# Kernel optimization log

Measured on AMD Instinct MI355X. Metric: run time of the kernel, lower is better.

Reference implementation:

```python
import jax, jax.numpy as jnp
import numpy as np

ALPHA = 0.1
NUM_CLASSES = 1000
B, D = 16384, 2048


def setup_inputs() -> dict:
    key = jax.random.key(0)
    k1, k2 = jax.random.split(key)
    x = jax.random.normal(k1, (B, D), dtype=jnp.float32)
    y = jax.random.randint(k2, (B,), 0, NUM_CLASSES)
    return {"x": x, "y": y}


def reference(x, y):
    # Per-class mean/std via a single segment reduction (equivalent to the
    # original masked loop over classes; torch .std(0) is unbiased, ddof=1).
    cnt = jax.ops.segment_sum(jnp.ones((x.shape[0],), x.dtype), y, num_segments=NUM_CLASSES)  # [C]
    s = jax.ops.segment_sum(x, y, num_segments=NUM_CLASSES)        # [C, D]
    sq = jax.ops.segment_sum(x * x, y, num_segments=NUM_CLASSES)   # [C, D]
    cnt_ = cnt[:, None]
    mean = s / cnt_
    var = (sq - cnt_ * mean * mean) / (cnt_ - 1.0)  # unbiased variance
    std = jnp.sqrt(jnp.maximum(var, 0.0))
    nk, pk = jax.random.split(jax.random.key(42))
    # torch.normal(mean, std).detach()
    class_noise = jax.lax.stop_gradient(mean + std * jax.random.normal(nk, mean.shape, x.dtype))
    index = jax.random.permutation(pk, x.shape[0])
    newY = y[index]
    out = (1.0 - ALPHA) * x + ALPHA * class_noise[newY]
    return out, newY
```

## Files before the change

### kernel.cpp

```cpp
#include <hip/hip_runtime.h>
#include <cstdint>
#include <cstddef>

#define B_ROWS 16384
#define D_COLS 2048
#define NCLS   1000

__host__ __device__ __forceinline__ uint32_t rotl32(uint32_t v, int r) {
    return (v << r) | (v >> (32 - r));
}

__host__ __device__ inline void tf2x32(uint32_t k0, uint32_t k1,
                                       uint32_t x0, uint32_t x1,
                                       uint32_t& o0, uint32_t& o1) {
    uint32_t ks0 = k0, ks1 = k1, ks2 = k0 ^ k1 ^ 0x1BD11BDAu;
    x0 += ks0; x1 += ks1;
    x0 += x1; x1 = rotl32(x1, 13); x1 ^= x0;
    x0 += x1; x1 = rotl32(x1, 15); x1 ^= x0;
    x0 += x1; x1 = rotl32(x1, 26); x1 ^= x0;
    x0 += x1; x1 = rotl32(x1, 6);  x1 ^= x0;
    x0 += ks1; x1 += ks2 + 1u;
    x0 += x1; x1 = rotl32(x1, 17); x1 ^= x0;
    x0 += x1; x1 = rotl32(x1, 29); x1 ^= x0;
    x0 += x1; x1 = rotl32(x1, 16); x1 ^= x0;
    x0 += x1; x1 = rotl32(x1, 24); x1 ^= x0;
    x0 += ks2; x1 += ks0 + 2u;
    x0 += x1; x1 = rotl32(x1, 13); x1 ^= x0;
    x0 += x1; x1 = rotl32(x1, 15); x1 ^= x0;
    x0 += x1; x1 = rotl32(x1, 26); x1 ^= x0;
    x0 += x1; x1 = rotl32(x1, 6);  x1 ^= x0;
    x0 += ks0; x1 += ks1 + 3u;
    x0 += x1; x1 = rotl32(x1, 17); x1 ^= x0;
    x0 += x1; x1 = rotl32(x1, 29); x1 ^= x0;
    x0 += x1; x1 = rotl32(x1, 16); x1 ^= x0;
    x0 += x1; x1 = rotl32(x1, 24); x1 ^= x0;
    x0 += ks1; x1 += ks2 + 4u;
    x0 += x1; x1 = rotl32(x1, 13); x1 ^= x0;
    x0 += x1; x1 = rotl32(x1, 15); x1 ^= x0;
    x0 += x1; x1 = rotl32(x1, 26); x1 ^= x0;
    x0 += x1; x1 = rotl32(x1, 6);  x1 ^= x0;
    x0 += ks2; x1 += ks0 + 5u;
    o0 = x0; o1 = x1;
}

__device__ __forceinline__ float erfinv_f(float x) {
    float w = -log1pf(-x * x);
    float p;
    if (w < 5.0f) {
        w -= 2.5f;
        p = 2.81022636e-08f;
        p = fmaf(p, w, 3.43273939e-07f);
        p = fmaf(p, w, -3.5233877e-06f);
        p = fmaf(p, w, -4.39150654e-06f);
        p = fmaf(p, w, 0.00021858087f);
        p = fmaf(p, w, -0.00125372503f);
        p = fmaf(p, w, -0.00417768164f);
        p = fmaf(p, w, 0.246640727f);
        p = fmaf(p, w, 1.50140941f);
    } else {
        w = sqrtf(w) - 3.0f;
        p = -0.000200214257f;
        p = fmaf(p, w, 0.000100950558f);
        p = fmaf(p, w, 0.00134934322f);
        p = fmaf(p, w, -0.00367342844f);
        p = fmaf(p, w, 0.00573950773f);
        p = fmaf(p, w, -0.0076224613f);
        p = fmaf(p, w, 0.00943887047f);
        p = fmaf(p, w, 1.00167406f);
        p = fmaf(p, w, 2.83297682f);
    }
    return p * x;
}


__global__ void k_bits_hist(const int* __restrict__ y, int* __restrict__ cnt,
                            unsigned long long* __restrict__ kA,
                            unsigned long long* __restrict__ kB,
                            uint32_t s1_0, uint32_t s1_1,
                            uint32_t s2_0, uint32_t s2_1) {
    int i = blockIdx.x * 256 + threadIdx.x;
    atomicAdd(&cnt[y[i]], 1);
    uint32_t a, b;
    tf2x32(s1_0, s1_1, 0u, (uint32_t)i, a, b);
    kA[i] = ((unsigned long long)(a ^ b) << 14) | (unsigned)i;
    tf2x32(s2_0, s2_1, 0u, (uint32_t)i, a, b);
    kB[i] = ((unsigned long long)(a ^ b) << 14) | (unsigned)i;
}

__global__ void k_prefix(const int* __restrict__ cnt, int* __restrict__ rowstart) {
    __shared__ int sm[1024];
    int t = threadIdx.x;
    int v = (t < NCLS) ? cnt[t] : 0;
    sm[t] = v;
    for (int off = 1; off < 1024; off <<= 1) {
        __syncthreads();
        int u = (t >= off) ? sm[t - off] : 0;
        __syncthreads();
        sm[t] += u;
    }
    if (t < NCLS) rowstart[t] = sm[t] - v;
}

__global__ void k_scatter_rows(const int* __restrict__ y, const int* __restrict__ rowstart,
                               int* __restrict__ rowpos, int* __restrict__ rowlist) {
    int i = blockIdx.x * 256 + threadIdx.x;
    int c = y[i];
    int p = atomicAdd(&rowpos[c], 1);
    rowlist[rowstart[c] + p] = i;
}

__global__ void __launch_bounds__(256) k_class_sums(
        const float* __restrict__ x, const int* __restrict__ rowlist,
        const int* __restrict__ rowstart, const int* __restrict__ cnt,
        float* __restrict__ s, float* __restrict__ sq) {
    int c = blockIdx.x, h = blockIdx.y, t = threadIdx.x;
    int start = rowstart[c], n = cnt[c];
    const float4* xb = (const float4*)x + (size_t)h * 256 + t;
    float sx=0,sy=0,sz=0,sw=0, qx=0,qy=0,qz=0,qw=0;
    int r = 0;
    for (; r + 2 <= n; r += 2) {
        int row0 = rowlist[start + r];
        int row1 = rowlist[start + r + 1];
        float4 a = xb[(size_t)row0 * 512];
        float4 b = xb[(size_t)row1 * 512];
        sx += a.x; sy += a.y; sz += a.z; sw += a.w;
        qx = fmaf(a.x, a.x, qx); qy = fmaf(a.y, a.y, qy);
        qz = fmaf(a.z, a.z, qz); qw = fmaf(a.w, a.w, qw);
        sx += b.x; sy += b.y; sz += b.z; sw += b.w;
        qx = fmaf(b.x, b.x, qx); qy = fmaf(b.y, b.y, qy);
        qz = fmaf(b.z, b.z, qz); qw = fmaf(b.w, b.w, qw);
    }
    if (r < n) {
        int row = rowlist[start + r];
        float4 a = xb[(size_t)row * 512];
        sx += a.x; sy += a.y; sz += a.z; sw += a.w;
        qx = fmaf(a.x, a.x, qx); qy = fmaf(a.y, a.y, qy);
        qz = fmaf(a.z, a.z, qz); qw = fmaf(a.w, a.w, qw);
    }
    int o = c * 512 + h * 256 + t;
    ((float4*)s)[o]  = make_float4(sx, sy, sz, sw);
    ((float4*)sq)[o] = make_float4(qx, qy, qz, qw);
}

__global__ void k_noise(const float* __restrict__ s, const float* __restrict__ sq,
                        const int* __restrict__ cnt, float* __restrict__ noise,
                        uint32_t nk0, uint32_t nk1) {
    int n = blockIdx.x * 256 + threadIdx.x;
    uint32_t b1, b2;
    tf2x32(nk0, nk1, 0u, (uint32_t)n, b1, b2);
    uint32_t bits = b1 ^ b2;
    float f = __uint_as_float((bits >> 9) | 0x3f800000u) - 1.0f;
    const float LO = -0.99999994f;
    float u = fmaxf(LO, fmaf(f, 2.0f, LO));
    float nr = 1.41421356f * erfinv_f(u);
    int c = n >> 11;
    float cf = (float)cnt[c];
    float m = s[n] / cf;
    float var = (sq[n] - cf * m * m) / (cf - 1.0f);
    float sd = sqrtf(fmaxf(var, 0.0f));
    noise[n] = fmaf(sd, nr, m);
}

__global__ void __launch_bounds__(256) k_rank12(
        const unsigned long long* __restrict__ kA,
        const unsigned long long* __restrict__ kB,
        int* __restrict__ rankA, int* __restrict__ rankB) {
    __shared__ unsigned long long sA[1024];
    __shared__ unsigned long long sB[1024];
    int t = threadIdx.x;
    int jbase = blockIdx.y * 1024;
    for (int k = t; k < 1024; k += 256) {
        sA[k] = kA[jbase + k];
        sB[k] = kB[jbase + k];
    }
    __syncthreads();
    int i0 = blockIdx.x * 512 + t;
    int i1 = i0 + 256;
    unsigned long long a0 = kA[i0], a1 = kA[i1];
    unsigned long long b0 = kB[i0], b1 = kB[i1];
    int ca0=0, ca1=0, cb0=0, cb1=0;
#pragma unroll 8
    for (int j = 0; j < 1024; j++) {
        unsigned long long sa = sA[j], sb = sB[j];
        ca0 += (sa < a0); ca1 += (sa < a1);
        cb0 += (sb < b0); cb1 += (sb < b1);
    }
    atomicAdd(&rankA[i0], ca0); atomicAdd(&rankA[i1], ca1);
    atomicAdd(&rankB[i0], cb0); atomicAdd(&rankB[i1], cb1);
}

__global__ void k_scatter1(const int* __restrict__ rank1, int* __restrict__ x1) {
    int i = blockIdx.x * 256 + threadIdx.x;
    x1[rank1[i]] = i;
}

__global__ void k_scatter2(const int* __restrict__ y, const int* __restrict__ x1,
                           const int* __restrict__ rank2, int* __restrict__ newY,
                           float* __restrict__ outTail) {
    int i = blockIdx.x * 256 + threadIdx.x;
    int v = y[x1[i]];
    int j = rank2[i];
    newY[j] = v;
    outTail[j] = (float)v;
}

__global__ void __launch_bounds__(256) k_final(
        const float* __restrict__ x, const float* __restrict__ noise,
        const int* __restrict__ newY, float* __restrict__ out) {
    int b = blockIdx.x, t = threadIdx.x;
    int ny = newY[b];
    const float4* xr = (const float4*)x + (size_t)b * (D_COLS / 4);
    const float4* nr = (const float4*)noise + (size_t)ny * (D_COLS / 4);
    float4* orow = (float4*)out + (size_t)b * (D_COLS / 4);
    float4 xa = xr[t], na = nr[t];
    float4 o;
    o.x = fmaf(0.1f, na.x, 0.9f * xa.x);
    o.y = fmaf(0.1f, na.y, 0.9f * xa.y);
    o.z = fmaf(0.1f, na.z, 0.9f * xa.z);
    o.w = fmaf(0.1f, na.w, 0.9f * xa.w);
    orow[t] = o;
    xa = xr[t + 256]; na = nr[t + 256];
    o.x = fmaf(0.1f, na.x, 0.9f * xa.x);
    o.y = fmaf(0.1f, na.y, 0.9f * xa.y);
    o.z = fmaf(0.1f, na.z, 0.9f * xa.z);
    o.w = fmaf(0.1f, na.w, 0.9f * xa.w);
    orow[t + 256] = o;
}

extern "C" void kernel_launch(void* const* d_in, const int* in_sizes, int n_in,
                              void* d_out, int out_size, void* d_ws, size_t ws_size,
                              hipStream_t stream) {
    const float* x = (const float*)d_in[0];
    const int* y = (const int*)d_in[1];
    float* out = (float*)d_out;
    float* outTail = out + (size_t)B_ROWS * D_COLS;

    char* ws = (char*)d_ws;
    float* s     = (float*)(ws);
    float* sq    = (float*)(ws + 8192000);
    float* noise = (float*)(ws + 16384000);
    unsigned long long* kA = (unsigned long long*)(ws + 24576000);
    unsigned long long* kB = (unsigned long long*)(ws + 24707072);
    int* ints = (int*)(ws + 24838144);
    int* cnt      = ints;
    int* rowpos   = ints + 1000;
    int* rank1    = ints + 2000;
    int* rank2    = ints + 18384;
    int* rowstart = ints + 34768;
    int* rowlist  = ints + 35768;
    int* x1       = ints + 52152;
    int* newY     = ints + 68536;

    hipMemsetAsync(cnt, 0, 34768 * sizeof(int), stream);

    uint32_t nk0, nk1, pk0, pk1, pn0, pn1, s1_0, s1_1, s2_0, s2_1;
    tf2x32(0u, 42u, 0u, 0u, nk0, nk1);
    tf2x32(0u, 42u, 0u, 1u, pk0, pk1);
    tf2x32(pk0, pk1, 0u, 0u, pn0, pn1);
    tf2x32(pk0, pk1, 0u, 1u, s1_0, s1_1);
    tf2x32(pn0, pn1, 0u, 1u, s2_0, s2_1);

    k_bits_hist<<<64, 256, 0, stream>>>(y, cnt, kA, kB, s1_0, s1_1, s2_0, s2_1);
    k_prefix<<<1, 1024, 0, stream>>>(cnt, rowstart);
    k_scatter_rows<<<64, 256, 0, stream>>>(y, rowstart, rowpos, rowlist);
    k_class_sums<<<dim3(NCLS, 2), 256, 0, stream>>>(x, rowlist, rowstart, cnt, s, sq);
    k_noise<<<8000, 256, 0, stream>>>(s, sq, cnt, noise, nk0, nk1);
    k_rank12<<<dim3(32, 16), 256, 0, stream>>>(kA, kB, rank1, rank2);
    k_scatter1<<<64, 256, 0, stream>>>(rank1, x1);
    k_scatter2<<<64, 256, 0, stream>>>(y, x1, rank2, newY, outTail);
    k_final<<<16384, 256, 0, stream>>>(x, noise, newY, out);
}
```

Before: 348.8 us.

## Replace all-pairs rank sort with bucketed counting sort for permutation

The permutation keys are now bucketed by their top 10 bits using a histogram, prefix sum and scatter, and each element is ranked only against the members of its own bucket, with ties broken by index. This replaces the O(N^2) all-pairs comparison kernel, which had to be followed by a separate scatter. Histogram atomics are added to the existing kernels and the prefix kernel is generalised to three blocks. The per-bucket rank loops are short (about 16 elements on average) but use scattered global loads.

```diff
diff --git a/kernel.cpp b/kernel.cpp
--- a/kernel.cpp
+++ b/kernel.cpp
@@ -5,6 +5,7 @@
 #define B_ROWS 16384
 #define D_COLS 2048
 #define NCLS   1000
+#define NBUCK  1024
 
 __host__ __device__ __forceinline__ uint32_t rotl32(uint32_t v, int r) {
     return (v << r) | (v >> (32 - r));
@@ -74,23 +75,33 @@
 
 
 __global__ void k_bits_hist(const int* __restrict__ y, int* __restrict__ cnt,
-                            unsigned long long* __restrict__ kA,
-                            unsigned long long* __restrict__ kB,
+                            uint32_t* __restrict__ kAbits, uint32_t* __restrict__ kBbits,
+                            int* __restrict__ bhA, int* __restrict__ bhB,
                             uint32_t s1_0, uint32_t s1_1,
                             uint32_t s2_0, uint32_t s2_1) {
     int i = blockIdx.x * 256 + threadIdx.x;
     atomicAdd(&cnt[y[i]], 1);
     uint32_t a, b;
     tf2x32(s1_0, s1_1, 0u, (uint32_t)i, a, b);
-    kA[i] = ((unsigned long long)(a ^ b) << 14) | (unsigned)i;
+    uint32_t bitsA = a ^ b;
+    kAbits[i] = bitsA;
+    atomicAdd(&bhA[bitsA >> 22], 1);
     tf2x32(s2_0, s2_1, 0u, (uint32_t)i, a, b);
-    kB[i] = ((unsigned long long)(a ^ b) << 14) | (unsigned)i;
-}
-
-__global__ void k_prefix(const int* __restrict__ cnt, int* __restrict__ rowstart) {
+    uint32_t bitsB = a ^ b;
+    kBbits[i] = bitsB;
+    atomicAdd(&bhB[bitsB >> 22], 1);
+}
+
+__global__ void k_prefix3(const int* __restrict__ cnt, int* __restrict__ rowstart,
+                          const int* __restrict__ bhA, int* __restrict__ bsA,
+                          const int* __restrict__ bhB, int* __restrict__ bsB) {
     __shared__ int sm[1024];
     int t = threadIdx.x;
-    int v = (t < NCLS) ? cnt[t] : 0;
+    const int* src; int* dst; int n;
+    if (blockIdx.x == 0)      { src = cnt; dst = rowstart; n = NCLS; }
+    else if (blockIdx.x == 1) { src = bhA; dst = bsA;      n = NBUCK; }
+    else                      { src = bhB; dst = bsB;      n = NBUCK; }
+    int v = (t < n) ? src[t] : 0;
     sm[t] = v;
     for (int off = 1; off < 1024; off <<= 1) {
         __syncthreads();
@@ -98,15 +109,28 @@
         __syncthreads();
         sm[t] += u;
     }
-    if (t < NCLS) rowstart[t] = sm[t] - v;
-}
-
-__global__ void k_scatter_rows(const int* __restrict__ y, const int* __restrict__ rowstart,
-                               int* __restrict__ rowpos, int* __restrict__ rowlist) {
+    if (t < n) dst[t] = sm[t] - v;
+}
+
+__global__ void k_scatter_all(const int* __restrict__ y,
+                              const uint32_t* __restrict__ kAbits,
+                              const uint32_t* __restrict__ kBbits,
+                              const int* __restrict__ rowstart, int* __restrict__ rowpos,
+                              int* __restrict__ rowlist,
+                              const int* __restrict__ bsA, int* __restrict__ bposA,
+                              int* __restrict__ memA,
+                              const int* __restrict__ bsB, int* __restrict__ bposB,
+                              int* __restrict__ memB) {
     int i = blockIdx.x * 256 + threadIdx.x;
     int c = y[i];
     int p = atomicAdd(&rowpos[c], 1);
     rowlist[rowstart[c] + p] = i;
+    uint32_t bA = kAbits[i] >> 22;
+    p = atomicAdd(&bposA[bA], 1);
+    memA[bsA[bA] + p] = i;
+    uint32_t bB = kBbits[i] >> 22;
+    p = atomicAdd(&bposB[bB], 1);
+    memB[bsB[bB] + p] = i;
 }
 
 __global__ void __launch_bounds__(256) k_class_sums(
@@ -161,37 +185,38 @@
     noise[n] = fmaf(sd, nr, m);
 }
 
-__global__ void __launch_bounds__(256) k_rank12(
-        const unsigned long long* __restrict__ kA,
-        const unsigned long long* __restrict__ kB,
-        int* __restrict__ rankA, int* __restrict__ rankB) {
-    __shared__ unsigned long long sA[1024];
-    __shared__ unsigned long long sB[1024];
-    int t = threadIdx.x;
-    int jbase = blockIdx.y * 1024;
-    for (int k = t; k < 1024; k += 256) {
-        sA[k] = kA[jbase + k];
-        sB[k] = kB[jbase + k];
-    }
-    __syncthreads();
-    int i0 = blockIdx.x * 512 + t;
-    int i1 = i0 + 256;
-    unsigned long long a0 = kA[i0], a1 = kA[i1];
-    unsigned long long b0 = kB[i0], b1 = kB[i1];
-    int ca0=0, ca1=0, cb0=0, cb1=0;
-#pragma unroll 8
-    for (int j = 0; j < 1024; j++) {
-        unsigned long long sa = sA[j], sb = sB[j];
-        ca0 += (sa < a0); ca1 += (sa < a1);
-        cb0 += (sb < b0); cb1 += (sb < b1);
-    }
-    atomicAdd(&rankA[i0], ca0); atomicAdd(&rankA[i1], ca1);
-    atomicAdd(&rankB[i0], cb0); atomicAdd(&rankB[i1], cb1);
-}
-
-__global__ void k_scatter1(const int* __restrict__ rank1, int* __restrict__ x1) {
+__global__ void k_rankAB(const uint32_t* __restrict__ kAbits,
+                         const uint32_t* __restrict__ kBbits,
+                         const int* __restrict__ bsA, const int* __restrict__ bhA,
+                         const int* __restrict__ memA,
+                         const int* __restrict__ bsB, const int* __restrict__ bhB,
+                         const int* __restrict__ memB,
+                         int* __restrict__ x1, int* __restrict__ rank2) {
     int i = blockIdx.x * 256 + threadIdx.x;
-    x1[rank1[i]] = i;
+    uint32_t a = kAbits[i];
+    {
+        uint32_t b = a >> 22;
+        int st = bsA[b], n = bhA[b];
+        int ca = 0;
+        for (int k = 0; k < n; k++) {
+            int m = memA[st + k];
+            uint32_t mb = kAbits[m];
+            ca += (mb < a) || (mb == a && m < i);
+        }
+        x1[st + ca] = i;
+    }
+    uint32_t c = kBbits[i];
+    {
+        uint32_t b = c >> 22;
+        int st = bsB[b], n = bhB[b];
+        int cb = 0;
+        for (int k = 0; k < n; k++) {
+            int m = memB[st + k];
+            uint32_t mb = kBbits[m];
+            cb += (mb < c) || (mb == c && m < i);
+        }
+        rank2[i] = st + cb;
+    }
 }
 
 __global__ void k_scatter2(const int* __restrict__ y, const int* __restrict__ x1,
@@ -239,19 +264,26 @@
     float* s     = (float*)(ws);
     float* sq    = (float*)(ws + 8192000);
     float* noise = (float*)(ws + 16384000);
-    unsigned long long* kA = (unsigned long long*)(ws + 24576000);
-    unsigned long long* kB = (unsigned long long*)(ws + 24707072);
-    int* ints = (int*)(ws + 24838144);
+    int* ints = (int*)(ws + 24576000);
     int* cnt      = ints;
     int* rowpos   = ints + 1000;
-    int* rank1    = ints + 2000;
-    int* rank2    = ints + 18384;
-    int* rowstart = ints + 34768;
-    int* rowlist  = ints + 35768;
-    int* x1       = ints + 52152;
-    int* newY     = ints + 68536;
-
-    hipMemsetAsync(cnt, 0, 34768 * sizeof(int), stream);
+    int* bhA      = ints + 2000;
+    int* bposA    = ints + 3024;
+    int* bhB      = ints + 4048;
+    int* bposB    = ints + 5072;
+    int* rowstart = ints + 6096;
+    int* bsA      = ints + 7096;
+    int* bsB      = ints + 8120;
+    int* rowlist  = ints + 9144;
+    int* memA     = ints + 25528;
+    int* memB     = ints + 41912;
+    int* x1       = ints + 58296;
+    int* rank2    = ints + 74680;
+    int* newY     = ints + 91064;
+    uint32_t* kAbits = (uint32_t*)(ints + 107448);
+    uint32_t* kBbits = (uint32_t*)(ints + 123832);
+
+    hipMemsetAsync(cnt, 0, 6096 * sizeof(int), stream);
 
     uint32_t nk0, nk1, pk0, pk1, pn0, pn1, s1_0, s1_1, s2_0, s2_1;
     tf2x32(0u, 42u, 0u, 0u, nk0, nk1);
@@ -260,13 +292,16 @@
     tf2x32(pk0, pk1, 0u, 1u, s1_0, s1_1);
     tf2x32(pn0, pn1, 0u, 1u, s2_0, s2_1);
 
-    k_bits_hist<<<64, 256, 0, stream>>>(y, cnt, kA, kB, s1_0, s1_1, s2_0, s2_1);
-    k_prefix<<<1, 1024, 0, stream>>>(cnt, rowstart);
-    k_scatter_rows<<<64, 256, 0, stream>>>(y, rowstart, rowpos, rowlist);
+    k_bits_hist<<<64, 256, 0, stream>>>(y, cnt, kAbits, kBbits, bhA, bhB,
+                                        s1_0, s1_1, s2_0, s2_1);
+    k_prefix3<<<3, 1024, 0, stream>>>(cnt, rowstart, bhA, bsA, bhB, bsB);
+    k_scatter_all<<<64, 256, 0, stream>>>(y, kAbits, kBbits, rowstart, rowpos,
+                                          rowlist, bsA, bposA, memA,
+                                          bsB, bposB, memB);
     k_class_sums<<<dim3(NCLS, 2), 256, 0, stream>>>(x, rowlist, rowstart, cnt, s, sq);
     k_noise<<<8000, 256, 0, stream>>>(s, sq, cnt, noise, nk0, nk1);
-    k_rank12<<<dim3(32, 16), 256, 0, stream>>>(kA, kB, rank1, rank2);
-    k_scatter1<<<64, 256, 0, stream>>>(rank1, x1);
+    k_rankAB<<<64, 256, 0, stream>>>(kAbits, kBbits, bsA, bhA, memA,
+                                     bsB, bhB, memB, x1, rank2);
     k_scatter2<<<64, 256, 0, stream>>>(y, x1, rank2, newY, outTail);
     k_final<<<16384, 256, 0, stream>>>(x, noise, newY, out);
 }
```

After: 322.8 us. 7.4% less time.
